# Kernel optimization log

Measured on AMD Instinct MI355X. Metric: run time of the kernel, lower is better.

The kernel has to match this reference:

```python
import jax, jax.numpy as jnp
import numpy as np
import math

D_MODEL = 768
H = 12
D_FF = 3072
HEAD_DIM = D_MODEL // H
EPS = 1e-5


def setup_inputs() -> dict:
    key = jax.random.key(0)
    ks = jax.random.split(key, 12)
    s = 1.0 / math.sqrt(D_MODEL)
    inp = {
        "x": jax.random.normal(ks[0], (8, 1024, D_MODEL), dtype=jnp.float32),
        # attention projections (stored as [d_in, d_out])
        "wq": jax.random.normal(ks[1], (D_MODEL, D_MODEL), jnp.float32) * s,
        "bq": jnp.zeros((D_MODEL,), jnp.float32),
        "wk": jax.random.normal(ks[2], (D_MODEL, D_MODEL), jnp.float32) * s,
        "bk": jnp.zeros((D_MODEL,), jnp.float32),
        "wv": jax.random.normal(ks[3], (D_MODEL, D_MODEL), jnp.float32) * s,
        "bv": jnp.zeros((D_MODEL,), jnp.float32),
        "wo": jax.random.normal(ks[4], (D_MODEL, D_MODEL), jnp.float32) * s,
        "bo": jnp.zeros((D_MODEL,), jnp.float32),
        # FFN
        "w1": jax.random.normal(ks[5], (D_MODEL, D_FF), jnp.float32) * s,
        "b1": jnp.zeros((D_FF,), jnp.float32),
        "w2": jax.random.normal(ks[6], (D_FF, D_MODEL), jnp.float32) * (1.0 / math.sqrt(D_FF)),
        "b2": jnp.zeros((D_MODEL,), jnp.float32),
        # LayerNormalization scalar params (gemma/beta) for the two residual norms
        "g1": jnp.ones((1,), jnp.float32),
        "be1": jnp.zeros((1,), jnp.float32),
        "g2": jnp.ones((1,), jnp.float32),
        "be2": jnp.zeros((1,), jnp.float32),
    }
    return inp


def _layernorm(x, g, b):
    # torch: mean and UNBIASED std over last dim; divide by (std + eps)
    mean = jnp.mean(x, axis=-1, keepdims=True)
    std = jnp.std(x, axis=-1, keepdims=True, ddof=1)
    return g * (x - mean) / (std + EPS) + b


def _attention(x, wq, bq, wk, bk, wv, bv, wo, bo):
    B, N, _ = x.shape
    q = (x @ wq + bq).reshape(B, N, H, HEAD_DIM)
    k = (x @ wk + bk).reshape(B, N, H, HEAD_DIM)
    v = (x @ wv + bv).reshape(B, N, H, HEAD_DIM)
    scores = jnp.einsum("bqhd,bkhd->bhqk", q, k) / math.sqrt(HEAD_DIM)
    w = jax.nn.softmax(scores, axis=-1)
    out = jnp.einsum("bhqk,bkhd->bqhd", w, v).reshape(B, N, D_MODEL)
    return out @ wo + bo


def _ffn(x, w1, b1, w2, b2):
    return (jax.nn.gelu(x @ w1 + b1, approximate=False)) @ w2 + b2


def reference(x, wq, bq, wk, bk, wv, bv, wo, bo, w1, b1, w2, b2, g1, be1, g2, be2):
    # pre-LN residual block 1: attention
    x = x + _attention(_layernorm(x, g1, be1), wq, bq, wk, bk, wv, bv, wo, bo)
    # pre-LN residual block 2: FFN
    x = x + _ffn(_layernorm(x, g2, be2), w1, b1, w2, b2)
    return x
```

## Files before the change

kernel.cpp:

```cpp
#include <hip/hip_runtime.h>
#include <hip/hip_bf16.h>
#include <math.h>

typedef unsigned short u16;
typedef unsigned int u32;
typedef u16 u16x8 __attribute__((ext_vector_type(8)));
typedef __bf16 bf16x8 __attribute__((ext_vector_type(8)));
typedef float f32x4 __attribute__((ext_vector_type(4)));

#define MODE_GELU 1
#define MODE_QKV 3

template <typename T, typename F>
__device__ __forceinline__ T bitcast(F f) { return __builtin_bit_cast(T, f); }

__device__ __forceinline__ u16 f2bf(float f) {
    unsigned int u = __float_as_uint(f);
    u = (u + 0x7fffu + ((u >> 16) & 1u)) >> 16;
    return (u16)u;
}

__device__ __forceinline__ float bf2f(u16 u) {
    return __uint_as_float(((u32)u) << 16);
}

__device__ __forceinline__ u32 packbf(float lo, float hi) {
    return (u32)f2bf(lo) | ((u32)f2bf(hi) << 16);
}

__device__ __forceinline__ float fast_gelu(float x) {
    const float arg = x * (2.30220775f + 0.10294329f * x * x);
    const float e = exp2f(arg);
    return x * (1.0f - __builtin_amdgcn_rcpf(e + 1.0f));
}

__device__ __forceinline__ void gl_lds16(const u16* g, u16* l) {
    __builtin_amdgcn_global_load_lds(
        (const __attribute__((address_space(1))) unsigned int*)(const void*)g,
        (__attribute__((address_space(3))) unsigned int*)(void*)l,
        16, 0, 0);
}

__device__ __forceinline__ void stage64(const u16* __restrict__ src, int stride,
                                        u16* __restrict__ lds, int t)
{
    const int wave = t >> 6, lane = t & 63;
#pragma unroll
    for (int i = 0; i < 2; i++) {
        const int row = i * 32 + wave * 8 + (lane >> 3);
        const int s = lane & 7;
        const int f = (((row >> 3) & 1) << 2) | (row & 3);
        gl_lds16(src + (size_t)row * stride + (size_t)((s ^ f) << 3),
                 lds + i * 2048 + wave * 512);
    }
}

__device__ __forceinline__ void stage64w8(const u16* __restrict__ src, int stride,
                                          u16* __restrict__ lds, int t)
{
    const int wave = t >> 6, lane = t & 63;
    const int row = wave * 8 + (lane >> 3);
    const int s = lane & 7;
    const int f = (((row >> 3) & 1) << 2) | (row & 3);
    gl_lds16(src + (size_t)row * stride + (size_t)((s ^ f) << 3),
             lds + wave * 512);
}

__global__ __launch_bounds__(256) void prep_kernel(
    const float* __restrict__ wq, const float* __restrict__ wk,
    const float* __restrict__ wv, const float* __restrict__ wo,
    const float* __restrict__ w1, const float* __restrict__ w2,
    const float* __restrict__ bq, const float* __restrict__ bk,
    const float* __restrict__ bv,
    u16* __restrict__ wqkvT, u16* __restrict__ woT,
    u16* __restrict__ w1T, u16* __restrict__ w2T, float* __restrict__ bqkv,
    const float* __restrict__ X, u16* __restrict__ Y,
    const float* __restrict__ gp, const float* __restrict__ bp)
{
    const int blk = blockIdx.x;
    if (blk >= 6921) {
        __shared__ float sbuf[8];
        const int row = blk - 6921, t = threadIdx.x;
        const float* xr = X + (size_t)row * 768;
        float v0 = xr[t], v1 = xr[t + 256], v2 = xr[t + 512];
        float s = v0 + v1 + v2;
        float q = v0 * v0 + v1 * v1 + v2 * v2;
#pragma unroll
        for (int m = 1; m < 64; m <<= 1) {
            s += __shfl_xor(s, m, 64);
            q += __shfl_xor(q, m, 64);
        }
        const int wave = t >> 6, lane = t & 63;
        if (lane == 0) { sbuf[wave] = s; sbuf[4 + wave] = q; }
        __syncthreads();
        s = sbuf[0] + sbuf[1] + sbuf[2] + sbuf[3];
        q = sbuf[4] + sbuf[5] + sbuf[6] + sbuf[7];
        const float mean = s * (1.0f / 768.0f);
        float ssd = fmaxf(q - 768.0f * mean * mean, 0.0f);
        const float stdv = sqrtf(ssd * (1.0f / 767.0f));
        const float scale = gp[0] / (stdv + 1e-5f);
        const float beta = bp[0];
        u16* yr = Y + (size_t)row * 768;
        yr[t]       = f2bf((v0 - mean) * scale + beta);
        yr[t + 256] = f2bf((v1 - mean) * scale + beta);
        yr[t + 512] = f2bf((v2 - mean) * scale + beta);
        return;
    }
    if (blk >= 6912) {
        const int t = (blk - 6912) * 256 + threadIdx.x;
        if (t < 2304)
            bqkv[t] = t < 768 ? bq[t] : (t < 1536 ? bk[t - 768] : bv[t - 1536]);
        return;
    }
    const float* W; u16* WT; int Krows, Ncols, lt;
    if (blk < 576)       { W = wq; WT = wqkvT;                       Krows = 768;  Ncols = 768;  lt = blk; }
    else if (blk < 1152) { W = wk; WT = wqkvT + (size_t)768 * 768;   Krows = 768;  Ncols = 768;  lt = blk - 576; }
    else if (blk < 1728) { W = wv; WT = wqkvT + (size_t)1536 * 768;  Krows = 768;  Ncols = 768;  lt = blk - 1152; }
    else if (blk < 2304) { W = wo; WT = woT;                         Krows = 768;  Ncols = 768;  lt = blk - 1728; }
    else if (blk < 4608) { W = w1; WT = w1T;                         Krows = 768;  Ncols = 3072; lt = blk - 2304; }
    else                 { W = w2; WT = w2T;                         Krows = 3072; Ncols = 768;  lt = blk - 4608; }
    const int ktiles = Krows >> 5;
    const int k0 = (lt % ktiles) * 32, n0 = (lt / ktiles) * 32;

    __shared__ float tile[32][33];
    const int tx = threadIdx.x & 31, ty = threadIdx.x >> 5;
#pragma unroll
    for (int j = 0; j < 32; j += 8)
        tile[ty + j][tx] = W[(size_t)(k0 + ty + j) * Ncols + n0 + tx];
    __syncthreads();
#pragma unroll
    for (int j = 0; j < 32; j += 8)
        WT[(size_t)(n0 + ty + j) * Krows + k0 + tx] = f2bf(tile[tx][ty + j]);
}

__global__ __launch_bounds__(256) void ln_bf16_kernel(
    const u16* __restrict__ X, u16* __restrict__ Y,
    const float* __restrict__ gp, const float* __restrict__ bp)
{
    __shared__ float sbuf[8];
    const int row = blockIdx.x, t = threadIdx.x;
    const u16* xr = X + (size_t)row * 768;
    float v0 = bf2f(xr[t]), v1 = bf2f(xr[t + 256]), v2 = bf2f(xr[t + 512]);
    float s = v0 + v1 + v2;
    float q = v0 * v0 + v1 * v1 + v2 * v2;
#pragma unroll
    for (int m = 1; m < 64; m <<= 1) {
        s += __shfl_xor(s, m, 64);
        q += __shfl_xor(q, m, 64);
    }
    const int wave = t >> 6, lane = t & 63;
    if (lane == 0) { sbuf[wave] = s; sbuf[4 + wave] = q; }
    __syncthreads();
    s = sbuf[0] + sbuf[1] + sbuf[2] + sbuf[3];
    q = sbuf[4] + sbuf[5] + sbuf[6] + sbuf[7];
    const float mean = s * (1.0f / 768.0f);
    float ssd = fmaxf(q - 768.0f * mean * mean, 0.0f);
    const float stdv = sqrtf(ssd * (1.0f / 767.0f));
    const float scale = gp[0] / (stdv + 1e-5f);
    const float beta = bp[0];
    u16* yr = Y + (size_t)row * 768;
    yr[t]       = f2bf((v0 - mean) * scale + beta);
    yr[t + 256] = f2bf((v1 - mean) * scale + beta);
    yr[t + 512] = f2bf((v2 - mean) * scale + beta);
}

template <int MODE>
__global__ __launch_bounds__(512) void gemm8w_kernel(
    const u16* __restrict__ A, const u16* __restrict__ BT,
    const float* __restrict__ bias,
    void* __restrict__ out0, void* __restrict__ out1, void* __restrict__ out2,
    int M, int N, int K)
{
    __shared__ u16 sh[2][2][128 * 64];
    u16* shp = &sh[0][0][0];
    const int t = threadIdx.x;
    const int lane = t & 63, wave = t >> 6;
    const int wr = wave >> 2, wc = wave & 3;
    const int g = lane >> 4, c = lane & 15;

    const int lin = blockIdx.x + blockIdx.y * gridDim.x;
    const int xcd = lin & 7, idx = lin >> 3;
    const int bm = xcd * 8 + (idx & 7);
    const int bn = idx >> 3;

    const int srow = t >> 3;
    const int sf = (((t >> 6) & 1) << 2) | ((t >> 3) & 3);
    const int sxor = ((t & 7) ^ sf) << 3;
    const u16* Ag = A + (size_t)(bm * 128 + srow) * K + sxor;
    const u16* Bg = BT + (size_t)(bn * 128 + srow) * K + sxor;

    const int fc = (((c >> 3) & 1) << 2) | (c & 3);
    const int xs0 = (g ^ fc) << 3;
    const int xs1 = ((4 + g) ^ fc) << 3;

    f32x4 acc[4][2] = {};
    const int nk = K >> 6;

#define STAGE8(buf, k0)                                                       \
    {                                                                         \
        _Pragma("unroll")                                                     \
        for (int i = 0; i < 2; i++) {                                         \
            gl_lds16(Ag + (size_t)(i * 64) * K + (k0), &sh[buf][0][i * 4096 + wave * 512]); \
            gl_lds16(Bg + (size_t)(i * 64) * K + (k0), &sh[buf][1][i * 4096 + wave * 512]); \
        }                                                                     \
    }

    STAGE8(0, 0);
    __syncthreads();

    for (int ks = 0; ks < nk; ks++) {
        const int cur = ks & 1;
        if (ks + 1 < nk) STAGE8(cur ^ 1, (ks + 1) << 6);
        const u16* Asb = sh[cur][0];
        const u16* Bsb = sh[cur][1];
        __builtin_amdgcn_s_setprio(1);
#pragma unroll
        for (int kk = 0; kk < 2; kk++) {
            const int xo = kk ? xs1 : xs0;
            bf16x8 af[4], bfr[2];
#pragma unroll
            for (int m = 0; m < 4; m++)
                af[m] = *(const bf16x8*)&Asb[(wr * 64 + m * 16 + c) * 64 + xo];
#pragma unroll
            for (int n = 0; n < 2; n++)
                bfr[n] = *(const bf16x8*)&Bsb[(wc * 32 + n * 16 + c) * 64 + xo];
#pragma unroll
            for (int m = 0; m < 4; m++)
#pragma unroll
                for (int n = 0; n < 2; n++)
                    acc[m][n] = __builtin_amdgcn_mfma_f32_16x16x32_bf16(
                        af[m], bfr[n], acc[m][n], 0, 0, 0);
        }
        __builtin_amdgcn_s_setprio(0);
        __syncthreads();
    }
#undef STAGE8

    if constexpr (MODE == MODE_QKV) {
        if (bn >= 12) {
#pragma unroll
            for (int m = 0; m < 4; m++) {
#pragma unroll
                for (int n = 0; n < 2; n++) {
                    const int colL = wc * 32 + n * 16 + c;
                    const int rowLb = wr * 64 + m * 16 + 4 * g;
                    const float bv = bias[bn * 128 + colL];
                    const u32 x0 = packbf(acc[m][n][0] + bv, acc[m][n][1] + bv);
                    const u32 x1 = packbf(acc[m][n][2] + bv, acc[m][n][3] + bv);
                    const int elem = colL * 128 + (rowLb ^ ((colL & 15) << 3));
                    ((u32*)shp)[elem >> 1] = x0;
                    ((u32*)shp)[(elem >> 1) + 1] = x1;
                }
            }
            __syncthreads();
            const int bn_off = bn - 12;
            const int bb = bm >> 3, kvb = (bm & 7) * 128;
            const int j8 = (t & 7) * 8;
#pragma unroll
            for (int it = 0; it < 2; it++) {
                const int colL2 = it * 64 + (t >> 3);
                const int gcol = bn_off * 128 + colL2;
                const int hh = gcol >> 6, d = gcol & 63;
                const size_t obase = ((size_t)(bb * 12 + hh) << 16) + ((size_t)d << 10) + kvb;
                const int X = (colL2 & 15) << 3;
#pragma unroll
                for (int half = 0; half < 2; half++) {
                    const int rowL2 = half * 64 + j8;
                    const int elem = colL2 * 128 + (rowL2 ^ X);
                    *(u16x8*)((u16*)out2 + obase + rowL2) = *(const u16x8*)&shp[elem];
                }
            }
            return;
        }
    }

#pragma unroll
    for (int m = 0; m < 4; m++) {
        const int row = bm * 128 + wr * 64 + m * 16 + 4 * g;
#pragma unroll
        for (int n = 0; n < 2; n++) {
            const int col = bn * 128 + wc * 32 + n * 16 + c;
            const float bv = bias[col];
#pragma unroll
            for (int i = 0; i < 4; i++) {
                float v = acc[m][n][i] + bv;
                if constexpr (MODE == MODE_GELU) {
                    ((u16*)out0)[(size_t)(row + i) * N + col] = f2bf(fast_gelu(v));
                } else {
                    const int sect = (col >= 768) ? 1 : 0;
                    const int colm = col - sect * 768;
                    u16* dst = sect ? (u16*)out1 : (u16*)out0;
                    dst[(size_t)(row + i) * 768 + colm] = f2bf(v);
                }
            }
        }
    }
}

template <int RES_BF16>
__global__ __launch_bounds__(256) void gemm64_kernel(
    const u16* __restrict__ A, const u16* __restrict__ BT,
    const float* __restrict__ bias, const void* __restrict__ res,
    void* __restrict__ out0, int M, int N, int K)
{
    __shared__ u16 sh[2][3][64 * 64];
    const int t = threadIdx.x;
    const int lane = t & 63, wave = t >> 6;
    const int g = lane >> 4, c = lane & 15;

    const int lin = blockIdx.x + blockIdx.y * gridDim.x;
    const int xcd = lin & 7, idx = lin >> 3;
    const int bm = xcd * 16 + (idx & 15);
    const int bn = idx >> 4;

    const u16* Ag = A + (size_t)(bm * 64) * K;
    const u16* Bg = BT + (size_t)(bn * 128) * K;

    const int fc = (((c >> 3) & 1) << 2) | (c & 3);
    const int xs0 = (g ^ fc) << 3;
    const int xs1 = ((4 + g) ^ fc) << 3;

    f32x4 acc[4][2] = {};
    const int nk = K >> 6;

#define STAGE64_AB(buf, k0)                                                   \
    {                                                                         \
        stage64(Ag + (k0), K, &sh[buf][0][0], t);                             \
        stage64(Bg + (k0), K, &sh[buf][1][0], t);                             \
        stage64(Bg + (size_t)64 * K + (k0), K, &sh[buf][2][0], t);            \
    }

    STAGE64_AB(0, 0);
    __syncthreads();

    for (int ks = 0; ks < nk; ks++) {
        const int cur = ks & 1;
        if (ks + 1 < nk) STAGE64_AB(cur ^ 1, (ks + 1) << 6);
        const u16* Asb = sh[cur][0];
        const u16* Bb = sh[cur][1 + (wave >> 1)];
        const int brow = (wave & 1) * 32;
        __builtin_amdgcn_s_setprio(1);
#pragma unroll
        for (int kk = 0; kk < 2; kk++) {
            const int xo = kk ? xs1 : xs0;
            bf16x8 af[4], bfr[2];
#pragma unroll
            for (int m = 0; m < 4; m++)
                af[m] = *(const bf16x8*)&Asb[(m * 16 + c) * 64 + xo];
#pragma unroll
            for (int n = 0; n < 2; n++)
                bfr[n] = *(const bf16x8*)&Bb[(brow + n * 16 + c) * 64 + xo];
#pragma unroll
            for (int m = 0; m < 4; m++)
#pragma unroll
                for (int n = 0; n < 2; n++)
                    acc[m][n] = __builtin_amdgcn_mfma_f32_16x16x32_bf16(
                        af[m], bfr[n], acc[m][n], 0, 0, 0);
        }
        __builtin_amdgcn_s_setprio(0);
        __syncthreads();
    }
#undef STAGE64_AB

#pragma unroll
    for (int m = 0; m < 4; m++) {
        const int row = bm * 64 + m * 16 + 4 * g;
#pragma unroll
        for (int n = 0; n < 2; n++) {
            const int col = bn * 128 + wave * 32 + n * 16 + c;
            const float bv = bias[col];
#pragma unroll
            for (int i = 0; i < 4; i++) {
                const size_t idxo = (size_t)(row + i) * N + col;
                if constexpr (RES_BF16 == 0) {
                    const float r = ((const float*)res)[idxo];
                    ((u16*)out0)[idxo] = f2bf(acc[m][n][i] + bv + r);
                } else {
                    const float r = bf2f(((const u16*)res)[idxo]);
                    ((float*)out0)[idxo] = acc[m][n][i] + bv + r;
                }
            }
        }
    }
}

__global__ __launch_bounds__(512) void attn_kernel(
    const u16* __restrict__ Qg, const u16* __restrict__ Kg,
    const u16* __restrict__ Vt_g, u16* __restrict__ O)
{
    __shared__ u16 Kl[2][4096];
    __shared__ u16 Vl[2][4096];
    const int t = threadIdx.x, lane = t & 63, wave = t >> 6;
    const int g = lane >> 4, c = lane & 15;
    const int l = blockIdx.x;
    const int pos = l >> 3;
    const int b = l & 7, h = pos >> 3;
    const int qt = pos & 7;
    const int bh = b * 12 + h;
    const size_t rowb = (size_t)b * 1024;
    const int q0 = qt * 128 + wave * 16;

    bf16x8 qa[2];
    {
        const u16* qp = Qg + (rowb + q0 + c) * 768 + h * 64 + g * 8;
        u16x8 a0 = *(const u16x8*)qp;
        u16x8 a1 = *(const u16x8*)(qp + 32);
        bf16x8 va0, va1;
#pragma unroll
        for (int j = 0; j < 8; j++) {
            const float SC = 0.18033688011112042f;
            va0[j] = (__bf16)(bf2f(a0[j]) * SC);
            va1[j] = (__bf16)(bf2f(a1[j]) * SC);
        }
        qa[0] = va0; qa[1] = va1;
    }

    bf16x8 vone;
#pragma unroll
    for (int j = 0; j < 8; j++) vone[j] = (__bf16)1.0f;

    int kro[4], kxo[4], vro[4];
#pragma unroll
    for (int n = 0; n < 4; n++) {
        const int pr = ((n >> 1) << 5) + ((c >> 2) << 3) + ((n & 1) << 2) + (c & 3);
        kro[n] = pr << 6;
        kxo[n] = (((pr >> 3) & 1) << 2) | (pr & 3);
        vro[n] = (n * 16 + c) << 6;
    }
    const int vxo = (((c >> 3) & 1) << 2) | (c & 3);

    const u16* ksrc = Kg + rowb * 768 + h * 64;
    const u16* vsrc = Vt_g + (size_t)bh * 65536;

    f32x4 oa[4] = {};
    f32x4 lsum = {};

    stage64w8(ksrc, 768, Kl[0], t);
    stage64w8(vsrc, 1024, Vl[0], t);
    __syncthreads();

    for (int kvt = 0; kvt < 16; ++kvt) {
        const u16* Kc = Kl[kvt & 1];
        const u16* Vc = Vl[kvt & 1];
        if (kvt < 15) {
            stage64w8(ksrc + (size_t)(kvt + 1) * 64 * 768, 768, Kl[(kvt + 1) & 1], t);
            stage64w8(vsrc + (kvt + 1) * 64, 1024, Vl[(kvt + 1) & 1], t);
        }

        f32x4 s0[4] = {};
        __builtin_amdgcn_s_setprio(1);
#pragma unroll
        for (int n = 0; n < 4; n++) {
#pragma unroll
            for (int kk = 0; kk < 2; kk++) {
                const bf16x8 kf = *(const bf16x8*)&Kc[kro[n] + ((((kk << 2) + g) ^ kxo[n]) << 3)];
                s0[n] = __builtin_amdgcn_mfma_f32_16x16x32_bf16(kf, qa[kk], s0[n], 0, 0, 0);
            }
        }
        __builtin_amdgcn_s_setprio(0);

        bf16x8 pa00, pa01;
#pragma unroll
        for (int n = 0; n < 4; n++)
#pragma unroll
            for (int i = 0; i < 4; i++)
                s0[n][i] = exp2f(fminf(s0[n][i], 60.0f));
#pragma unroll
        for (int i = 0; i < 4; i++) {
            pa00[i] = (__bf16)s0[0][i]; pa00[4 + i] = (__bf16)s0[1][i];
            pa01[i] = (__bf16)s0[2][i]; pa01[4 + i] = (__bf16)s0[3][i];
        }

        __builtin_amdgcn_s_setprio(1);
        lsum = __builtin_amdgcn_mfma_f32_16x16x32_bf16(pa00, vone, lsum, 0, 0, 0);
        lsum = __builtin_amdgcn_mfma_f32_16x16x32_bf16(pa01, vone, lsum, 0, 0, 0);
#pragma unroll
        for (int n = 0; n < 4; n++) {
#pragma unroll
            for (int kk = 0; kk < 2; kk++) {
                const bf16x8 vf = *(const bf16x8*)&Vc[vro[n] + ((((kk << 2) + g) ^ vxo) << 3)];
                oa[n] = __builtin_amdgcn_mfma_f32_16x16x32_bf16(kk ? pa01 : pa00, vf, oa[n], 0, 0, 0);
            }
        }
        __builtin_amdgcn_s_setprio(0);
        __syncthreads();
    }

#pragma unroll
    for (int i = 0; i < 4; i++) {
        const float ia_ = 1.0f / fmaxf(lsum[i], 1e-30f);
        const size_t ra_ = rowb + q0 + 4 * g + i;
#pragma unroll
        for (int n = 0; n < 4; n++)
            O[ra_ * 768 + h * 64 + n * 16 + c] = f2bf(oa[n][i] * ia_);
    }
}

extern "C" void kernel_launch(void* const* d_in, const int* in_sizes, int n_in,
                              void* d_out, int out_size, void* d_ws, size_t ws_size,
                              hipStream_t stream)
{
    const float* x   = (const float*)d_in[0];
    const float* wq  = (const float*)d_in[1];
    const float* bq  = (const float*)d_in[2];
    const float* wk  = (const float*)d_in[3];
    const float* bk  = (const float*)d_in[4];
    const float* wv  = (const float*)d_in[5];
    const float* bv  = (const float*)d_in[6];
    const float* wo  = (const float*)d_in[7];
    const float* bo  = (const float*)d_in[8];
    const float* w1  = (const float*)d_in[9];
    const float* b1  = (const float*)d_in[10];
    const float* w2  = (const float*)d_in[11];
    const float* b2  = (const float*)d_in[12];
    const float* g1  = (const float*)d_in[13];
    const float* be1 = (const float*)d_in[14];
    const float* g2  = (const float*)d_in[15];
    const float* be2 = (const float*)d_in[16];

    char* ws = (char*)d_ws;
    constexpr size_t O_WQKV = 0;
    constexpr size_t O_WO   = 3538944;
    constexpr size_t O_W1   = 4718592;
    constexpr size_t O_W2   = 9437184;
    constexpr size_t O_BQKV = 14155776;
    constexpr size_t O_XLN  = 14168064;
    constexpr size_t O_Q    = O_XLN + 12582912;
    constexpr size_t O_K    = O_Q + 12582912;
    constexpr size_t O_VT   = O_K + 12582912;
    constexpr size_t O_ATTN = O_VT + 12582912;
    constexpr size_t O_H    = O_ATTN + 12582912;
    constexpr size_t O_F    = O_XLN;
    constexpr size_t O_HLN  = O_ATTN;

    u16* wqkvT = (u16*)(ws + O_WQKV);
    u16* woT   = (u16*)(ws + O_WO);
    u16* w1T   = (u16*)(ws + O_W1);
    u16* w2T   = (u16*)(ws + O_W2);
    float* bqkv = (float*)(ws + O_BQKV);
    u16* xln   = (u16*)(ws + O_XLN);
    u16* Qb    = (u16*)(ws + O_Q);
    u16* Kb    = (u16*)(ws + O_K);
    u16* VTg   = (u16*)(ws + O_VT);
    u16* attnb = (u16*)(ws + O_ATTN);
    u16* hB    = (u16*)(ws + O_H);
    u16* fb    = (u16*)(ws + O_F);
    u16* hln   = (u16*)(ws + O_HLN);

    dim3 blk(256);
    prep_kernel<<<6921 + 8192, blk, 0, stream>>>(wq, wk, wv, wo, w1, w2, bq, bk, bv,
                                                 wqkvT, woT, w1T, w2T, bqkv,
                                                 x, xln, g1, be1);
    gemm8w_kernel<MODE_QKV><<<dim3(64, 18), dim3(512), 0, stream>>>(
        xln, wqkvT, bqkv, Qb, Kb, VTg, 8192, 2304, 768);
    attn_kernel<<<768, dim3(512), 0, stream>>>(Qb, Kb, VTg, attnb);
    gemm64_kernel<0><<<dim3(128, 6), blk, 0, stream>>>(
        attnb, woT, bo, x, hB, 8192, 768, 768);
    ln_bf16_kernel<<<8192, blk, 0, stream>>>(hB, hln, g2, be2);
    gemm8w_kernel<MODE_GELU><<<dim3(64, 24), dim3(512), 0, stream>>>(
        hln, w1T, b1, fb, nullptr, nullptr, 8192, 3072, 768);
    gemm64_kernel<1><<<dim3(128, 6), blk, 0, stream>>>(
        fb, w2T, b2, hB, (float*)d_out, 8192, 768, 3072);
}
```

Measured before the change: 228.5 us.

## Replace FFN up-projection GEMM with 256x256-tile pipelined GELU kernel

Adds a dedicated 256x256 tile GEMM for the first FFN projection with fused bias and GELU, replacing the 128x128 8-wave kernel. It uses a double-buffered LDS schedule with interleaved global-to-LDS staging, explicit vmcnt waits and barriers, and raised wave priority around the MFMA blocks. The larger tiles are meant to raise data reuse per block and overlap loads with MFMA work. In exchange the kernel uses 128 KB of LDS and many accumulator registers, and runs only 384 blocks. The K loop is hardcoded for K=768.

Result: slower. 234.9 us (+2.8%).

```diff
diff --git a/kernel.cpp b/kernel.cpp
--- a/kernel.cpp
+++ b/kernel.cpp
@@ -293,6 +293,150 @@
                     dst[(size_t)(row + i) * 768 + colm] = f2bf(v);
                 }
             }
+        }
+    }
+}
+
+__global__ __launch_bounds__(512, 2) void gemm256_gelu(
+    const u16* __restrict__ A, const u16* __restrict__ BT,
+    const float* __restrict__ bias, u16* __restrict__ out0,
+    int M, int N, int K)
+{
+    __shared__ u16 sh[2][2][16384];
+    const int t = threadIdx.x, lane = t & 63, wave = t >> 6;
+    const int wr = wave >> 2, wc = wave & 3;
+    const int g = lane >> 4, c = lane & 15;
+
+    const int lin = blockIdx.x;
+    const int xcd = lin & 7, idx = lin >> 3;
+    const int bm = xcd * 4 + (idx & 3);
+    const int bn = idx >> 2;
+
+    const u16* Ag = A + (size_t)(bm * 256) * K;
+    const u16* Bg = BT + (size_t)(bn * 256) * K;
+
+    const int fc = (((c >> 3) & 1) << 2) | (c & 3);
+    const int sfA = (((t >> 6) & 1) << 2) | ((t >> 3) & 3);
+    const int sxA = ((t & 7) ^ sfA) << 3;
+    const int fB = ((wave & 1) << 2) | ((lane >> 3) & 3);
+    const int sxB = ((lane & 7) ^ fB) << 3;
+
+#define STG_A(ks, bi)                                                         \
+    gl_lds16(Ag + (size_t)((bi) * 64 + (t >> 3)) * K + (ks) * 64 + sxA,       \
+             &sh[(ks) & 1][0][(bi) * 4096 + wave * 512]);
+#define STG_B(ks, par, j)                                                     \
+    {                                                                         \
+        const int rb_ = ((j) * 4 + ((wave >> 2) << 1) + (par)) * 32 + (wave & 3) * 8; \
+        gl_lds16(Bg + (size_t)(rb_ + (lane >> 3)) * K + (ks) * 64 + sxB,      \
+                 &sh[(ks) & 1][1][rb_ * 64]);                                 \
+    }
+#define STG_H(ht, ks)                                                         \
+    {                                                                         \
+        if ((ht) == 0) { STG_A(ks, 0); STG_A(ks, 2); }                        \
+        else if ((ht) == 1) { STG_A(ks, 1); STG_A(ks, 3); }                   \
+        else { STG_B(ks, (ht) - 2, 0); STG_B(ks, (ht) - 2, 1); }              \
+    }
+
+    f32x4 acc[8][4] = {};
+    bf16x8 af[4][2], bf0[2][2], bf1[2][2];
+
+#define LDA(d, QR)                                                            \
+    _Pragma("unroll") for (int m = 0; m < 4; m++)                             \
+        _Pragma("unroll") for (int kk = 0; kk < 2; kk++)                      \
+            af[m][kk] = *(const bf16x8*)&sh[d][0][(wr * 128 + (QR) * 64 + m * 16 + c) * 64 + ((kk * 4 + g) ^ fc) * 8];
+#define LDB(d, QC, dst)                                                       \
+    _Pragma("unroll") for (int n = 0; n < 2; n++)                             \
+        _Pragma("unroll") for (int kk = 0; kk < 2; kk++)                      \
+            dst[n][kk] = *(const bf16x8*)&sh[d][1][(wc * 64 + (QC) * 32 + n * 16 + c) * 64 + ((kk * 4 + g) ^ fc) * 8];
+#define MFMA16(QR, QC, bsrc)                                                  \
+    __builtin_amdgcn_s_setprio(1);                                            \
+    _Pragma("unroll") for (int m = 0; m < 4; m++)                             \
+        _Pragma("unroll") for (int n = 0; n < 2; n++)                         \
+            _Pragma("unroll") for (int kk = 0; kk < 2; kk++)                  \
+                acc[(QR) * 4 + m][(QC) * 2 + n] = __builtin_amdgcn_mfma_f32_16x16x32_bf16( \
+                    af[m][kk], bsrc[n][kk], acc[(QR) * 4 + m][(QC) * 2 + n], 0, 0, 0); \
+    __builtin_amdgcn_s_setprio(0);
+#define FB(vm)                                                                \
+    asm volatile(vm ::: "memory");                                            \
+    __builtin_amdgcn_s_barrier();
+
+    STG_H(0, 0); STG_H(2, 0); STG_H(3, 0); STG_H(1, 0); STG_H(0, 1); STG_H(2, 1);
+    FB("s_waitcnt vmcnt(8)");
+
+    for (int it2 = 0; it2 < 5; ++it2) {
+        const int a = 2 * it2, b = a + 1;
+        LDA(0, 0); LDB(0, 0, bf0);
+        STG_H(1, b);
+        MFMA16(0, 0, bf0);
+        FB("s_waitcnt vmcnt(6)");
+        LDB(0, 1, bf1);
+        STG_H(3, b);
+        MFMA16(0, 1, bf1);
+        FB("");
+        LDA(0, 1);
+        STG_H(0, a + 2);
+        MFMA16(1, 0, bf0);
+        FB("");
+        STG_H(2, a + 2);
+        MFMA16(1, 1, bf1);
+        FB("s_waitcnt vmcnt(8)");
+        LDA(1, 0); LDB(1, 0, bf0);
+        STG_H(1, a + 2);
+        MFMA16(0, 0, bf0);
+        FB("s_waitcnt vmcnt(6)");
+        LDB(1, 1, bf1);
+        STG_H(3, a + 2);
+        MFMA16(0, 1, bf1);
+        FB("");
+        LDA(1, 1);
+        STG_H(0, b + 2);
+        MFMA16(1, 0, bf0);
+        FB("");
+        STG_H(2, b + 2);
+        MFMA16(1, 1, bf1);
+        FB("s_waitcnt vmcnt(8)");
+    }
+    {
+        LDA(0, 0); LDB(0, 0, bf0);
+        STG_H(1, 11);
+        MFMA16(0, 0, bf0);
+        FB("s_waitcnt vmcnt(6)");
+        LDB(0, 1, bf1);
+        STG_H(3, 11);
+        MFMA16(0, 1, bf1);
+        FB("");
+        LDA(0, 1);
+        MFMA16(1, 0, bf0);
+        FB("");
+        MFMA16(1, 1, bf1);
+        FB("s_waitcnt vmcnt(4)");
+        LDA(1, 0); LDB(1, 0, bf0);
+        MFMA16(0, 0, bf0);
+        FB("s_waitcnt vmcnt(0)");
+        LDB(1, 1, bf1);
+        MFMA16(0, 1, bf1);
+        LDA(1, 1);
+        MFMA16(1, 0, bf0);
+        MFMA16(1, 1, bf1);
+    }
+#undef FB
+#undef MFMA16
+#undef LDB
+#undef LDA
+#undef STG_H
+#undef STG_B
+#undef STG_A
+
+#pragma unroll
+    for (int qm = 0; qm < 8; qm++) {
+        const int row = bm * 256 + wr * 128 + qm * 16 + 4 * g;
+#pragma unroll
+        for (int qn = 0; qn < 4; qn++) {
+            const int col = bn * 256 + wc * 64 + qn * 16 + c;
+            const float bv = bias[col];
+#pragma unroll
+            for (int i = 0; i < 4; i++)
+                out0[(size_t)(row + i) * N + col] = f2bf(fast_gelu(acc[qm][qn][i] + bv));
         }
     }
 }
@@ -557,8 +701,8 @@
     gemm64_kernel<0><<<dim3(128, 6), blk, 0, stream>>>(
         attnb, woT, bo, x, hB, 8192, 768, 768);
     ln_bf16_kernel<<<8192, blk, 0, stream>>>(hB, hln, g2, be2);
-    gemm8w_kernel<MODE_GELU><<<dim3(64, 24), dim3(512), 0, stream>>>(
-        hln, w1T, b1, fb, nullptr, nullptr, 8192, 3072, 768);
+    gemm256_gelu<<<384, dim3(512), 0, stream>>>(
+        hln, w1T, b1, fb, 8192, 3072, 768);
     gemm64_kernel<1><<<dim3(128, 6), blk, 0, stream>>>(
         fb, w2T, b2, hB, (float*)d_out, 8192, 768, 3072);
 }
```
